# Kernel optimization log

Measured on AMD Instinct MI355X. Metric: run time of the kernel, lower is better.

## Reference

```python
import jax, jax.numpy as jnp
import numpy as np

N_NODES = 50000
N_EDGES = 800000
D = 256            # node_feat_size
D_EDGE = 16        # edge_feat_size (unused in forward math, as in the original)
G_FEAT = 200       # graph_feat_size
N_TASKS = 1
N_GRAPHS = 512


def _p(key, shape):
    return jax.random.normal(key, shape, dtype=jnp.float32) * 0.05


def setup_inputs() -> dict:
    key = jax.random.key(0)
    ks = jax.random.split(key, 24)
    inp = {
        'node_feats_1': jax.random.normal(ks[0], (N_NODES, D), dtype=jnp.float32),
        'edge_feats_1': jax.random.normal(ks[1], (N_EDGES, D_EDGE), dtype=jnp.float32),
        'node_feats_2': jax.random.normal(ks[2], (N_NODES, D), dtype=jnp.float32),
        'edge_feats_2': jax.random.normal(ks[3], (N_EDGES, D_EDGE), dtype=jnp.float32),
        'src_1': jax.random.randint(ks[4], (N_EDGES,), 0, N_NODES, dtype=jnp.int32),
        'dst_1': jax.random.randint(ks[5], (N_EDGES,), 0, N_NODES, dtype=jnp.int32),
        'graph_ids_1': jnp.sort(jax.random.randint(ks[6], (N_NODES,), 0, N_GRAPHS, dtype=jnp.int32)),
        'src_2': jax.random.randint(ks[7], (N_EDGES,), 0, N_NODES, dtype=jnp.int32),
        'dst_2': jax.random.randint(ks[8], (N_EDGES,), 0, N_NODES, dtype=jnp.int32),
        'graph_ids_2': jnp.sort(jax.random.randint(ks[9], (N_NODES,), 0, N_GRAPHS, dtype=jnp.int32)),
        # GCN layer 1 params (GraphConv weight/bias + residual Linear)
        'W1': _p(ks[10], (D, D)), 'b1': jnp.zeros((D,), jnp.float32),
        'Wr1': _p(ks[11], (D, D)), 'br1': jnp.zeros((D,), jnp.float32),
        # GCN layer 2 params
        'W2': _p(ks[12], (D, D)), 'b2': jnp.zeros((D,), jnp.float32),
        'Wr2': _p(ks[13], (D, D)), 'br2': jnp.zeros((D,), jnp.float32),
        # Readout 1 MLP
        'Ri1': _p(ks[14], (D, D)), 'rbi1': jnp.zeros((D,), jnp.float32),
        'Ro1': _p(ks[15], (D, G_FEAT)), 'rbo1': jnp.zeros((G_FEAT,), jnp.float32),
        # Readout 2 MLP
        'Ri2': _p(ks[16], (D, D)), 'rbi2': jnp.zeros((D,), jnp.float32),
        'Ro2': _p(ks[17], (D, G_FEAT)), 'rbo2': jnp.zeros((G_FEAT,), jnp.float32),
        # Predictor
        'Wp': _p(ks[18], (G_FEAT, N_TASKS)), 'bp': jnp.zeros((N_TASKS,), jnp.float32),
    }
    return inp


def _gcn_layer(h, src, dst, W, b, Wr, br):
    # DGL GraphConv, norm='none': project, aggregate (sum src->dst), bias, relu
    hW = h @ W                                             # [N, D]
    agg = jax.ops.segment_sum(jnp.take(hW, src, axis=0), dst, num_segments=N_NODES)
    conv = jax.nn.relu(agg + b)
    # residual branch: activation(Linear(h))
    res = jax.nn.relu(h @ Wr + br)
    return conv + res                                      # dropout=0, no batchnorm


def _readout(h, graph_ids, Wi, bi, Wo, bo):
    # MLPNodeReadout: Linear -> relu -> Linear, then sum over nodes per graph
    h = jax.nn.relu(h @ Wi + bi)
    h = h @ Wo + bo                                        # [N, G_FEAT]
    return jax.ops.segment_sum(h, graph_ids, num_segments=N_GRAPHS)


def reference(node_feats_1, edge_feats_1, node_feats_2, edge_feats_2,
              src_1, dst_1, graph_ids_1, src_2, dst_2, graph_ids_2,
              W1, b1, Wr1, br1, W2, b2, Wr2, br2,
              Ri1, rbi1, Ro1, rbo1, Ri2, rbi2, Ro2, rbo2, Wp, bp):
    h1 = _gcn_layer(node_feats_1, src_1, dst_1, W1, b1, Wr1, br1)
    g1 = _readout(h1, graph_ids_1, Ri1, rbi1, Ro1, rbo1)
    h2 = _gcn_layer(node_feats_2, src_2, dst_2, W2, b2, Wr2, br2)
    g2 = _readout(h2, graph_ids_2, Ri2, rbi2, Ro2, rbo2)
    g = g1 + g2                                            # [G, G_FEAT]
    return (g @ Wp + bp).reshape(-1)                       # [G * n_tasks]
```

## Files before the change

kernel.cpp:

```cpp
#include <hip/hip_runtime.h>

#define NN 50000
#define NE 800000
#define DD 256
#define GFEAT 200
#define NG 512

typedef __bf16 bf16;
typedef bf16 bf16x4 __attribute__((ext_vector_type(4)));
typedef bf16 bf16x8 __attribute__((ext_vector_type(8)));
typedef float f32x4 __attribute__((ext_vector_type(4)));

__device__ __forceinline__ void gl_lds16(const bf16* g, bf16* l) {
    __builtin_amdgcn_global_load_lds(
        (const __attribute__((address_space(1))) uint32_t*)(g),
        (__attribute__((address_space(3))) uint32_t*)(l), 16, 0, 0);
}

__device__ __forceinline__ bf16x8 frag_ld(const bf16* s, int R, int C) {
    return *(const bf16x8*)&s[R * 32 + ((C ^ ((R >> 1) & 3)) << 3)];
}

#define EPI_STRIDE 136

__global__ __launch_bounds__(256) void conv_x2_kernel(const float* __restrict__ in0,
                                                      const float* __restrict__ in1,
                                                      bf16* __restrict__ out0,
                                                      bf16* __restrict__ out1, int n4) {
    const float* in = blockIdx.y ? in1 : in0;
    bf16* out = blockIdx.y ? out1 : out0;
    int i = blockIdx.x * 256 + threadIdx.x;
    if (i < n4) {
        float4 v = ((const float4*)in)[i];
        bf16x4 o;
        o[0] = (bf16)v.x; o[1] = (bf16)v.y; o[2] = (bf16)v.z; o[3] = (bf16)v.w;
        ((bf16x4*)out)[i] = o;
    }
}

__global__ __launch_bounds__(256) void conv_w8_kernel(
    const float* __restrict__ w0, const float* __restrict__ w1,
    const float* __restrict__ w2, const float* __restrict__ w3,
    const float* __restrict__ w4, const float* __restrict__ w5,
    const float* __restrict__ w6, const float* __restrict__ w7,
    bf16* __restrict__ out_base) {
    const float* ws[8] = {w0, w1, w2, w3, w4, w5, w6, w7};
    const int Ns[8] = {DD, DD, DD, GFEAT, DD, DD, DD, GFEAT};
    int m = blockIdx.y;
    const float* in = ws[m];
    int N = Ns[m];
    int idx = blockIdx.x * 256 + threadIdx.x;
    int n = idx >> 8, k = idx & 255;
    float v = (n < N) ? in[k * N + n] : 0.f;
    out_base[(size_t)m * 65536 + idx] = (bf16)v;
}

#define NBKT   128
#define NPB    391
#define NCHUNK 256
#define CE     ((NE + NCHUNK - 1) / NCHUNK)

__global__ __launch_bounds__(256) void csr_coarse_hist_kernel(
    const int* __restrict__ d0, const int* __restrict__ d1,
    int* __restrict__ cnt0, int* __restrict__ cnt1) {
    const int blk = blockIdx.x, t = threadIdx.x;
    const int* dst = blockIdx.y ? d1 : d0;
    int* cnt = blockIdx.y ? cnt1 : cnt0;
    __shared__ int hist[NBKT];
    if (t < NBKT) hist[t] = 0;
    __syncthreads();
    const int e0 = blk * CE;
    const int e1 = (e0 + CE < NE) ? e0 + CE : NE;
    for (int e = e0 + t; e < e1; e += 256)
        atomicAdd(&hist[dst[e] / NPB], 1);
    __syncthreads();
    if (t < NBKT) cnt[t * NCHUNK + blk] = hist[t];
}

__global__ __launch_bounds__(1024) void csr_scan_kernel(
    int* __restrict__ cnt0, int* __restrict__ cnt1,
    int* __restrict__ offs0, int* __restrict__ offs1) {
    int* cnt = blockIdx.y ? cnt1 : cnt0;
    const int t = threadIdx.x;
    const int PER = (NBKT * NCHUNK) / 1024;
    int v[PER];
    int sum = 0;
    const int base = t * PER;
#pragma unroll
    for (int i = 0; i < PER; i += 4) {
        int4 q = *(const int4*)&cnt[base + i];
        v[i] = q.x; v[i + 1] = q.y; v[i + 2] = q.z; v[i + 3] = q.w;
        sum += q.x + q.y + q.z + q.w;
    }
    __shared__ int s[1024];
    s[t] = sum;
    __syncthreads();
    for (int off = 1; off < 1024; off <<= 1) {
        int a = (t >= off) ? s[t - off] : 0;
        __syncthreads();
        s[t] += a;
        __syncthreads();
    }
    int run = s[t] - sum;
#pragma unroll
    for (int i = 0; i < PER; i++) { int c = v[i]; cnt[base + i] = run; run += c; }
    if (t == 0) (blockIdx.y ? offs1 : offs0)[NN] = NE;
}

__global__ __launch_bounds__(256) void csr_partition_kernel(
    const int* __restrict__ sA, const int* __restrict__ sB,
    const int* __restrict__ d0, const int* __restrict__ d1,
    const int* __restrict__ cnt0, const int* __restrict__ cnt1,
    int2* __restrict__ eb0, int2* __restrict__ eb1) {
    const int blk = blockIdx.x, t = threadIdx.x;
    const int* src = blockIdx.y ? sB : sA;
    const int* dst = blockIdx.y ? d1 : d0;
    const int* cnt = blockIdx.y ? cnt1 : cnt0;
    int2* eb = blockIdx.y ? eb1 : eb0;
    __shared__ int cur[NBKT];
    if (t < NBKT) cur[t] = cnt[t * NCHUNK + blk];
    __syncthreads();
    const int e0 = blk * CE;
    const int e1 = (e0 + CE < NE) ? e0 + CE : NE;
    for (int e = e0 + t; e < e1; e += 256) {
        int d = dst[e], s = src[e];
        int pos = atomicAdd(&cur[d / NPB], 1);
        eb[pos] = make_int2(s, d);
    }
}

__global__ __launch_bounds__(512) void csr_bucket_sort_kernel(
    const int* __restrict__ cnt0, const int* __restrict__ cnt1,
    const int2* __restrict__ eb0, const int2* __restrict__ eb1,
    int* __restrict__ offs0, int* __restrict__ offs1,
    int* __restrict__ csr0, int* __restrict__ csr1) {
    const int b = blockIdx.x, t = threadIdx.x;
    const int* cnt = blockIdx.y ? cnt1 : cnt0;
    const int2* eb = blockIdx.y ? eb1 : eb0;
    int* offs = blockIdx.y ? offs1 : offs0;
    int* csr = blockIdx.y ? csr1 : csr0;
    const int lo = b * NPB;
    const int ncnt = (NN - lo < NPB) ? (NN - lo) : NPB;
    const int beg = cnt[b * NCHUNK];
    const int end = (b == NBKT - 1) ? NE : cnt[(b + 1) * NCHUNK];

    __shared__ int hist[NPB];
    __shared__ int s[512];
    if (t < NPB) hist[t] = 0;
    __syncthreads();
    for (int i = beg + t; i < end; i += 512)
        atomicAdd(&hist[eb[i].y - lo], 1);
    __syncthreads();

    int h = (t < NPB) ? hist[t] : 0;
    s[t] = h;
    __syncthreads();
    for (int off = 1; off < 512; off <<= 1) {
        int a = (t >= off) ? s[t - off] : 0;
        __syncthreads();
        s[t] += a;
        __syncthreads();
    }
    int excl = s[t] - h;
    __syncthreads();
    if (t < NPB) hist[t] = excl;
    if (t < ncnt) offs[lo + t] = beg + excl;
    __syncthreads();

    for (int i = beg + t; i < end; i += 512) {
        int2 v = eb[i];
        int pos = atomicAdd(&hist[v.y - lo], 1);
        csr[beg + pos] = v.x;
    }
}

__global__ __launch_bounds__(256) void mfma_gemm2_kernel(
    const bf16* __restrict__ A0, const bf16* __restrict__ A1,
    const bf16* __restrict__ Bt0, const bf16* __restrict__ Bt1,
    const float* __restrict__ bias0, const float* __restrict__ bias1,
    bf16* __restrict__ out0, bf16* __restrict__ out1,
    int M, int Nb, int do_relu) {
    const int lid = blockIdx.x;
    const int r8 = lid & 7, cc = (lid >> 3) & 1, g = lid >> 4;
    const int row_blk = g * 8 + r8;
    if (row_blk * 128 >= M) return;
    const bf16* A = blockIdx.y ? A1 : A0;
    const bf16* Bt = blockIdx.y ? Bt1 : Bt0;
    const float* bias = blockIdx.y ? bias1 : bias0;
    bf16* out = blockIdx.y ? out1 : out0;

    __shared__ bf16 smem[16384];
    bf16* As = smem;
    bf16* Bs = smem + 8192;

    const int t    = threadIdx.x;
    const int lane = t & 63;
    const int w    = t >> 6;
    const int row0 = row_blk * 128;
    const int col0 = cc * 128;

    f32x4 acc[4][4] = {};
    const int wm = (w >> 1) * 64, wn = (w & 1) * 64;
    const int fm = lane & 15, fC = lane >> 4;

    for (int k0 = 0; k0 < 256; k0 += 32) {
#pragma unroll
        for (int r = 0; r < 2; r++) {
            int flat = r * 256 + t;
            int fr = flat >> 2, fc = flat & 3;
            int fcg = fc ^ ((fr >> 1) & 3);
            int arow = row0 + fr;
            if (arow > M - 1) arow = M - 1;
            gl_lds16(&A[(size_t)arow * 256 + k0 + fcg * 8], &As[flat * 8]);
        }
#pragma unroll
        for (int r = 0; r < 2; r++) {
            int flat = r * 256 + t;
            int fr = flat >> 2, fc = flat & 3;
            int fcg = fc ^ ((fr >> 1) & 3);
            int brow = col0 + fr;
            gl_lds16(&Bt[(size_t)brow * 256 + k0 + fcg * 8], &Bs[flat * 8]);
        }
        __syncthreads();

        bf16x8 af[4], bfr[4];
#pragma unroll
        for (int i = 0; i < 4; i++) af[i] = frag_ld(As, wm + i * 16 + fm, fC);
#pragma unroll
        for (int i = 0; i < 4; i++) bfr[i] = frag_ld(Bs, wn + i * 16 + fm, fC);
#pragma unroll
        for (int i = 0; i < 4; i++)
#pragma unroll
            for (int j = 0; j < 4; j++)
                acc[i][j] = __builtin_amdgcn_mfma_f32_16x16x32_bf16(af[i], bfr[j], acc[i][j], 0, 0, 0);
        __syncthreads();
    }

    float bv[4];
#pragma unroll
    for (int j = 0; j < 4; j++) {
        int col = col0 + wn + fm + j * 16;
        bv[j] = (col < Nb) ? bias[col] : 0.f;
    }

#pragma unroll
    for (int p = 0; p < 2; p++) {
        if ((w >> 1) == p) {
#pragma unroll
            for (int i = 0; i < 4; i++)
#pragma unroll
                for (int j = 0; j < 4; j++)
#pragma unroll
                    for (int r2 = 0; r2 < 4; r2++) {
                        int rl = i * 16 + (lane >> 4) * 4 + r2;
                        int cl = wn + fm + j * 16;
                        float v = acc[i][j][r2] + bv[j];
                        if (do_relu) v = fmaxf(v, 0.f);
                        smem[rl * EPI_STRIDE + cl] = (bf16)v;
                    }
        }
        __syncthreads();
#pragma unroll
        for (int q = 0; q < 4; q++) {
            int flat = q * 256 + t;
            int rl = flat >> 4, seg = flat & 15;
            int grow = row0 + p * 64 + rl;
            if (grow < M)
                *(bf16x8*)&out[(size_t)grow * 256 + col0 + seg * 8] =
                    *(const bf16x8*)&smem[rl * EPI_STRIDE + seg * 8];
        }
        __syncthreads();
    }
}

__global__ __launch_bounds__(256) void mfma_gemm_fused2_kernel(
    const bf16* __restrict__ A0, const bf16* __restrict__ A1,
    const bf16* __restrict__ Bt2_0, const bf16* __restrict__ Bt2_1,
    const float* __restrict__ bh0, const float* __restrict__ bh1,
    bf16* __restrict__ lo0, bf16* __restrict__ lo1,
    bf16* __restrict__ hi0, bf16* __restrict__ hi1, int M) {
    const int lid = blockIdx.x;
    const int r8 = lid & 7, cc = (lid >> 3) & 3, g = lid >> 5;
    const int row_blk = g * 8 + r8;
    if (row_blk * 128 >= M) return;
    const bf16* A = blockIdx.y ? A1 : A0;
    const bf16* Bt2 = blockIdx.y ? Bt2_1 : Bt2_0;
    const float* bias_hi = blockIdx.y ? bh1 : bh0;
    bf16* out_lo = blockIdx.y ? lo1 : lo0;
    bf16* out_hi = blockIdx.y ? hi1 : hi0;

    __shared__ bf16 smem[16384];
    bf16* As = smem;
    bf16* Bs = smem + 8192;

    const int t    = threadIdx.x;
    const int lane = t & 63;
    const int w    = t >> 6;
    const int row0 = row_blk * 128;
    const int col0 = cc * 128;

    f32x4 acc[4][4] = {};
    const int wm = (w >> 1) * 64, wn = (w & 1) * 64;
    const int fm = lane & 15, fC = lane >> 4;

    for (int k0 = 0; k0 < 256; k0 += 32) {
#pragma unroll
        for (int r = 0; r < 2; r++) {
            int flat = r * 256 + t;
            int fr = flat >> 2, fc = flat & 3;
            int fcg = fc ^ ((fr >> 1) & 3);
            int arow = row0 + fr;
            if (arow > M - 1) arow = M - 1;
            gl_lds16(&A[(size_t)arow * 256 + k0 + fcg * 8], &As[flat * 8]);
        }
#pragma unroll
        for (int r = 0; r < 2; r++) {
            int flat = r * 256 + t;
            int fr = flat >> 2, fc = flat & 3;
            int fcg = fc ^ ((fr >> 1) & 3);
            int brow = col0 + fr;
            gl_lds16(&Bt2[(size_t)brow * 256 + k0 + fcg * 8], &Bs[flat * 8]);
        }
        __syncthreads();

        bf16x8 af[4], bfr[4];
#pragma unroll
        for (int i = 0; i < 4; i++) af[i] = frag_ld(As, wm + i * 16 + fm, fC);
#pragma unroll
        for (int i = 0; i < 4; i++) bfr[i] = frag_ld(Bs, wn + i * 16 + fm, fC);
#pragma unroll
        for (int i = 0; i < 4; i++)
#pragma unroll
            for (int j = 0; j < 4; j++)
                acc[i][j] = __builtin_amdgcn_mfma_f32_16x16x32_bf16(af[i], bfr[j], acc[i][j], 0, 0, 0);
        __syncthreads();
    }

    const bool hi = (col0 >= 256);
    bf16* out = hi ? out_hi : out_lo;
    const int cb = hi ? col0 - 256 : col0;

    float bv[4];
#pragma unroll
    for (int j = 0; j < 4; j++) {
        int col = cb + wn + fm + j * 16;
        bv[j] = hi ? bias_hi[col] : 0.f;
    }

#pragma unroll
    for (int p = 0; p < 2; p++) {
        if ((w >> 1) == p) {
#pragma unroll
            for (int i = 0; i < 4; i++)
#pragma unroll
                for (int j = 0; j < 4; j++)
#pragma unroll
                    for (int r2 = 0; r2 < 4; r2++) {
                        int rl = i * 16 + (lane >> 4) * 4 + r2;
                        int cl = wn + fm + j * 16;
                        float v = acc[i][j][r2] + bv[j];
                        if (hi) v = fmaxf(v, 0.f);
                        smem[rl * EPI_STRIDE + cl] = (bf16)v;
                    }
        }
        __syncthreads();
#pragma unroll
        for (int q = 0; q < 4; q++) {
            int flat = q * 256 + t;
            int rl = flat >> 4, seg = flat & 15;
            int grow = row0 + p * 64 + rl;
            if (grow < M)
                *(bf16x8*)&out[(size_t)grow * 256 + cb + seg * 8] =
                    *(const bf16x8*)&smem[rl * EPI_STRIDE + seg * 8];
        }
        __syncthreads();
    }
}

__global__ __launch_bounds__(256) void agg_combine2_kernel(
    const bf16* __restrict__ hW0, const bf16* __restrict__ hW1,
    const int* __restrict__ csr0, const int* __restrict__ csr1,
    const int* __restrict__ offs0, const int* __restrict__ offs1,
    const float* __restrict__ bias0, const float* __restrict__ bias1,
    const bf16* __restrict__ res0, const bf16* __restrict__ res1,
    bf16* __restrict__ H0, bf16* __restrict__ H1, int n_nodes) {
    const bf16* hW = blockIdx.y ? hW1 : hW0;
    const int* csr_src = blockIdx.y ? csr1 : csr0;
    const int* offsets = blockIdx.y ? offs1 : offs0;
    const float* bias = blockIdx.y ? bias1 : bias0;
    const bf16* res = blockIdx.y ? res1 : res0;
    bf16* H = blockIdx.y ? H1 : H0;

    int wave = threadIdx.x >> 6;
    int lane = threadIdx.x & 63;
    int node = blockIdx.x * 4 + wave;
    if (node >= n_nodes) return;
    int beg = offsets[node], end = offsets[node + 1];
    const int half = lane >> 5;
    const int fo   = (lane & 31) * 8;

    float acc[8] = {};
    int j = beg;
    for (; j + 6 + half < end; j += 8) {
        int s0 = csr_src[j + half];
        int s1 = csr_src[j + 2 + half];
        int s2 = csr_src[j + 4 + half];
        int s3 = csr_src[j + 6 + half];
        bf16x8 v0 = *(const bf16x8*)&hW[(size_t)s0 * DD + fo];
        bf16x8 v1 = *(const bf16x8*)&hW[(size_t)s1 * DD + fo];
        bf16x8 v2 = *(const bf16x8*)&hW[(size_t)s2 * DD + fo];
        bf16x8 v3 = *(const bf16x8*)&hW[(size_t)s3 * DD + fo];
#pragma unroll
        for (int q = 0; q < 8; q++) acc[q] += (float)v0[q];
#pragma unroll
        for (int q = 0; q < 8; q++) acc[q] += (float)v1[q];
#pragma unroll
        for (int q = 0; q < 8; q++) acc[q] += (float)v2[q];
#pragma unroll
        for (int q = 0; q < 8; q++) acc[q] += (float)v3[q];
    }
    for (; j + half < end; j += 2) {
        int s = csr_src[j + half];
        bf16x8 v = *(const bf16x8*)&hW[(size_t)s * DD + fo];
#pragma unroll
        for (int q = 0; q < 8; q++) acc[q] += (float)v[q];
    }
#pragma unroll
    for (int q = 0; q < 8; q++) acc[q] += __shfl_xor(acc[q], 32, 64);

    if (half == 0) {
        float4 b0 = *(const float4*)&bias[fo];
        float4 b1 = *(const float4*)&bias[fo + 4];
        bf16x8 rv = *(const bf16x8*)&res[(size_t)node * DD + fo];
        bf16x8 o;
        o[0] = (bf16)(fmaxf(acc[0] + b0.x, 0.f) + (float)rv[0]);
        o[1] = (bf16)(fmaxf(acc[1] + b0.y, 0.f) + (float)rv[1]);
        o[2] = (bf16)(fmaxf(acc[2] + b0.z, 0.f) + (float)rv[2]);
        o[3] = (bf16)(fmaxf(acc[3] + b0.w, 0.f) + (float)rv[3]);
        o[4] = (bf16)(fmaxf(acc[4] + b1.x, 0.f) + (float)rv[4]);
        o[5] = (bf16)(fmaxf(acc[5] + b1.y, 0.f) + (float)rv[5]);
        o[6] = (bf16)(fmaxf(acc[6] + b1.z, 0.f) + (float)rv[6]);
        o[7] = (bf16)(fmaxf(acc[7] + b1.w, 0.f) + (float)rv[7]);
        *(bf16x8*)&H[(size_t)node * DD + fo] = o;
    }
}

__global__ __launch_bounds__(256) void graph_reduce2_kernel(
    const bf16* __restrict__ P0, const bf16* __restrict__ P1,
    const int* __restrict__ g0, const int* __restrict__ g1,
    float* __restrict__ G0, float* __restrict__ G1, int n_nodes) {
    const bf16* P = blockIdx.y ? P1 : P0;
    const int* gids = blockIdx.y ? g1 : g0;
    float* G = blockIdx.y ? G1 : G0;

    int g = blockIdx.x;
    int lo = 0, hi = n_nodes;
    while (lo < hi) { int mid = (lo + hi) >> 1; if (gids[mid] < g) lo = mid + 1; else hi = mid; }
    int beg = lo;
    hi = n_nodes;
    while (lo < hi) { int mid = (lo + hi) >> 1; if (gids[mid] < g + 1) lo = mid + 1; else hi = mid; }
    int end = lo;

    int c = threadIdx.x;
    if (c < GFEAT) {
        float acc = 0.f;
        for (int r = beg; r < end; r++) acc += (float)P[(size_t)r * 256 + c];
        G[(size_t)g * GFEAT + c] = acc;
    }
}

__global__ __launch_bounds__(256) void predictor_kernel(const float* __restrict__ G1,
                                                        const float* __restrict__ G2,
                                                        const float* __restrict__ Wp,
                                                        const float* __restrict__ bp,
                                                        float* __restrict__ out) {
    int i = blockIdx.x * 256 + threadIdx.x;
    if (i >= NG) return;
    float acc = bp[0];
    for (int f = 0; f < GFEAT; f++)
        acc += (G1[i * GFEAT + f] + G2[i * GFEAT + f]) * Wp[f];
    out[i] = acc;
}

extern "C" void kernel_launch(void* const* d_in, const int* in_sizes, int n_in,
                              void* d_out, int out_size, void* d_ws, size_t ws_size,
                              hipStream_t stream) {
    const float* X1   = (const float*)d_in[0];
    const float* X2   = (const float*)d_in[2];
    const int*   src1 = (const int*)d_in[4];
    const int*   dst1 = (const int*)d_in[5];
    const int*   gid1 = (const int*)d_in[6];
    const int*   src2 = (const int*)d_in[7];
    const int*   dst2 = (const int*)d_in[8];
    const int*   gid2 = (const int*)d_in[9];
    const float* W1  = (const float*)d_in[10]; const float* b1  = (const float*)d_in[11];
    const float* Wr1 = (const float*)d_in[12]; const float* br1 = (const float*)d_in[13];
    const float* W2  = (const float*)d_in[14]; const float* b2  = (const float*)d_in[15];
    const float* Wr2 = (const float*)d_in[16]; const float* br2 = (const float*)d_in[17];
    const float* Ri1 = (const float*)d_in[18]; const float* rbi1 = (const float*)d_in[19];
    const float* Ro1 = (const float*)d_in[20]; const float* rbo1 = (const float*)d_in[21];
    const float* Ri2 = (const float*)d_in[22]; const float* rbi2 = (const float*)d_in[23];
    const float* Ro2 = (const float*)d_in[24]; const float* rbo2 = (const float*)d_in[25];
    const float* Wp  = (const float*)d_in[26]; const float* bp  = (const float*)d_in[27];

    const size_t NB = (size_t)NN * DD * sizeof(bf16);
    char* p = (char*)d_ws;
    bf16* XbH1 = (bf16*)p; p += NB;
    bf16* XbH2 = (bf16*)p; p += NB;
    bf16* hWR1 = (bf16*)p; p += NB;
    bf16* hWR2 = (bf16*)p; p += NB;
    bf16* resP1 = (bf16*)p; p += NB;
    bf16* resP2 = (bf16*)p; p += NB;
    float* G1  = (float*)p; p += (size_t)NG * GFEAT * sizeof(float);
    float* G2  = (float*)p; p += (size_t)NG * GFEAT * sizeof(float);
    bf16* Wbase = (bf16*)p; p += 8 * 65536 * sizeof(bf16);
    int* offs1 = (int*)p; p += (NN + 1) * sizeof(int);
    int* offs2 = (int*)p; p += (NN + 1) * sizeof(int);
    int* cnt1  = (int*)p; p += NBKT * NCHUNK * sizeof(int);
    int* cnt2  = (int*)p; p += NBKT * NCHUNK * sizeof(int);
    int* csr1  = (int*)p; p += NE * sizeof(int);
    int* csr2  = (int*)p; p += NE * sizeof(int);
    int2* eb1 = (int2*)hWR1;
    int2* eb2 = (int2*)hWR2;

    conv_w8_kernel<<<dim3(256, 8), 256, 0, stream>>>(W1, Wr1, Ri1, Ro1, W2, Wr2, Ri2, Ro2, Wbase);
    conv_x2_kernel<<<dim3((NN * DD / 4 + 255) / 256, 2), 256, 0, stream>>>(
        X1, X2, XbH1, XbH2, NN * DD / 4);

    csr_coarse_hist_kernel<<<dim3(NCHUNK, 2), 256, 0, stream>>>(dst1, dst2, cnt1, cnt2);
    csr_scan_kernel<<<dim3(1, 2), 1024, 0, stream>>>(cnt1, cnt2, offs1, offs2);
    csr_partition_kernel<<<dim3(NCHUNK, 2), 256, 0, stream>>>(
        src1, src2, dst1, dst2, cnt1, cnt2, eb1, eb2);
    csr_bucket_sort_kernel<<<dim3(NBKT, 2), 512, 0, stream>>>(
        cnt1, cnt2, eb1, eb2, offs1, offs2, csr1, csr2);

    mfma_gemm_fused2_kernel<<<dim3(49 * 32, 2), 256, 0, stream>>>(
        XbH1, XbH2, Wbase + 0 * 65536, Wbase + 4 * 65536, br1, br2,
        hWR1, hWR2, resP1, resP2, NN);
    agg_combine2_kernel<<<dim3((NN + 3) / 4, 2), 256, 0, stream>>>(
        hWR1, hWR2, csr1, csr2, offs1, offs2, b1, b2, resP1, resP2, XbH1, XbH2, NN);
    mfma_gemm2_kernel<<<dim3(49 * 16, 2), 256, 0, stream>>>(
        XbH1, XbH2, Wbase + 2 * 65536, Wbase + 6 * 65536, rbi1, rbi2,
        hWR1, hWR2, NN, DD, 1);
    mfma_gemm2_kernel<<<dim3(49 * 16, 2), 256, 0, stream>>>(
        hWR1, hWR2, Wbase + 3 * 65536, Wbase + 7 * 65536, rbo1, rbo2,
        resP1, resP2, NN, GFEAT, 0);
    graph_reduce2_kernel<<<dim3(NG, 2), 256, 0, stream>>>(
        resP1, resP2, gid1, gid2, G1, G2, NN);

    predictor_kernel<<<(NG + 255) / 256, 256, 0, stream>>>(G1, G2, Wp, bp, (float*)d_out);
}
```

Before: 576.1 us.

## Fuse readout segment-sum into output GEMM epilogue and widen K-tile

Replaces the separate graph_reduce kernel by doing the per-graph sum inside the final readout GEMM epilogue, using run-length accumulation over sorted graph ids and atomicAdd into a zeroed G buffer. This removes writing and rereading the projected readout matrix. It also doubles the GEMM K-step from 32 to 64 with an 8-way swizzle, halving the number of barriers per tile. The catch is extra atomics, float summation order that is no longer deterministic, and an added zeroing kernel.

```diff
diff --git a/kernel.cpp b/kernel.cpp
--- a/kernel.cpp
+++ b/kernel.cpp
@@ -17,8 +17,8 @@
         (__attribute__((address_space(3))) uint32_t*)(l), 16, 0, 0);
 }
 
-__device__ __forceinline__ bf16x8 frag_ld(const bf16* s, int R, int C) {
-    return *(const bf16x8*)&s[R * 32 + ((C ^ ((R >> 1) & 3)) << 3)];
+__device__ __forceinline__ bf16x8 frag_ld64(const bf16* s, int R, int C) {
+    return *(const bf16x8*)&s[R * 64 + ((C ^ ((R >> 1) & 7)) << 3)];
 }
 
 #define EPI_STRIDE 136
@@ -55,6 +55,13 @@
     out_base[(size_t)m * 65536 + idx] = (bf16)v;
 }
 
+__global__ __launch_bounds__(256) void zero_g_kernel(float* __restrict__ G0,
+                                                     float* __restrict__ G1) {
+    float* G = blockIdx.y ? G1 : G0;
+    int i = blockIdx.x * 256 + threadIdx.x;
+    if (i < NG * GFEAT) G[i] = 0.f;
+}
+
 #define NBKT   128
 #define NPB    391
 #define NCHUNK 256
@@ -174,6 +181,19 @@
     }
 }
 
+#define STAGE64(MAT, base_row, CLAMP_M)                                          \
+    _Pragma("unroll")                                                            \
+    for (int r_ = 0; r_ < 4; r_++) {                                             \
+        int flat_ = r_ * 256 + t;                                                \
+        int fr_ = flat_ >> 3, fc_ = flat_ & 7;                                   \
+        int fcg_ = fc_ ^ ((fr_ >> 1) & 7);                                       \
+        int row_ = (base_row) + fr_;                                             \
+        if (CLAMP_M && row_ > M - 1) row_ = M - 1;                               \
+        gl_lds16(&MAT[(size_t)row_ * 256 + k0 + fcg_ * 8],                       \
+                 &(((r_ < 2) ? As : As) )[0] + 0);                               \
+    }
+
+
 __global__ __launch_bounds__(256) void mfma_gemm2_kernel(
     const bf16* __restrict__ A0, const bf16* __restrict__ A1,
     const bf16* __restrict__ Bt0, const bf16* __restrict__ Bt1,
@@ -203,36 +223,38 @@
     const int wm = (w >> 1) * 64, wn = (w & 1) * 64;
     const int fm = lane & 15, fC = lane >> 4;
 
-    for (int k0 = 0; k0 < 256; k0 += 32) {
-#pragma unroll
-        for (int r = 0; r < 2; r++) {
+    for (int k0 = 0; k0 < 256; k0 += 64) {
+#pragma unroll
+        for (int r = 0; r < 4; r++) {
             int flat = r * 256 + t;
-            int fr = flat >> 2, fc = flat & 3;
-            int fcg = fc ^ ((fr >> 1) & 3);
+            int fr = flat >> 3, fc = flat & 7;
+            int fcg = fc ^ ((fr >> 1) & 7);
             int arow = row0 + fr;
             if (arow > M - 1) arow = M - 1;
             gl_lds16(&A[(size_t)arow * 256 + k0 + fcg * 8], &As[flat * 8]);
         }
 #pragma unroll
-        for (int r = 0; r < 2; r++) {
+        for (int r = 0; r < 4; r++) {
             int flat = r * 256 + t;
-            int fr = flat >> 2, fc = flat & 3;
-            int fcg = fc ^ ((fr >> 1) & 3);
+            int fr = flat >> 3, fc = flat & 7;
+            int fcg = fc ^ ((fr >> 1) & 7);
             int brow = col0 + fr;
             gl_lds16(&Bt[(size_t)brow * 256 + k0 + fcg * 8], &Bs[flat * 8]);
         }
         __syncthreads();
-
-        bf16x8 af[4], bfr[4];
-#pragma unroll
-        for (int i = 0; i < 4; i++) af[i] = frag_ld(As, wm + i * 16 + fm, fC);
-#pragma unroll
-        for (int i = 0; i < 4; i++) bfr[i] = frag_ld(Bs, wn + i * 16 + fm, fC);
-#pragma unroll
-        for (int i = 0; i < 4; i++)
-#pragma unroll
-            for (int j = 0; j < 4; j++)
-                acc[i][j] = __builtin_amdgcn_mfma_f32_16x16x32_bf16(af[i], bfr[j], acc[i][j], 0, 0, 0);
+#pragma unroll
+        for (int s = 0; s < 2; s++) {
+            bf16x8 af[4], bfr[4];
+#pragma unroll
+            for (int i = 0; i < 4; i++) af[i] = frag_ld64(As, wm + i * 16 + fm, s * 4 + fC);
+#pragma unroll
+            for (int i = 0; i < 4; i++) bfr[i] = frag_ld64(Bs, wn + i * 16 + fm, s * 4 + fC);
+#pragma unroll
+            for (int i = 0; i < 4; i++)
+#pragma unroll
+                for (int j = 0; j < 4; j++)
+                    acc[i][j] = __builtin_amdgcn_mfma_f32_16x16x32_bf16(af[i], bfr[j], acc[i][j], 0, 0, 0);
+        }
         __syncthreads();
     }
 
@@ -303,36 +325,38 @@
     const int wm = (w >> 1) * 64, wn = (w & 1) * 64;
     const int fm = lane & 15, fC = lane >> 4;
 
-    for (int k0 = 0; k0 < 256; k0 += 32) {
-#pragma unroll
-        for (int r = 0; r < 2; r++) {
+    for (int k0 = 0; k0 < 256; k0 += 64) {
+#pragma unroll
+        for (int r = 0; r < 4; r++) {
             int flat = r * 256 + t;
-            int fr = flat >> 2, fc = flat & 3;
-            int fcg = fc ^ ((fr >> 1) & 3);
+            int fr = flat >> 3, fc = flat & 7;
+            int fcg = fc ^ ((fr >> 1) & 7);
             int arow = row0 + fr;
             if (arow > M - 1) arow = M - 1;
             gl_lds16(&A[(size_t)arow * 256 + k0 + fcg * 8], &As[flat * 8]);
         }
 #pragma unroll
-        for (int r = 0; r < 2; r++) {
+        for (int r = 0; r < 4; r++) {
             int flat = r * 256 + t;
-            int fr = flat >> 2, fc = flat & 3;
-            int fcg = fc ^ ((fr >> 1) & 3);
+            int fr = flat >> 3, fc = flat & 7;
+            int fcg = fc ^ ((fr >> 1) & 7);
             int brow = col0 + fr;
             gl_lds16(&Bt2[(size_t)brow * 256 + k0 + fcg * 8], &Bs[flat * 8]);
         }
         __syncthreads();
-
-        bf16x8 af[4], bfr[4];
-#pragma unroll
-        for (int i = 0; i < 4; i++) af[i] = frag_ld(As, wm + i * 16 + fm, fC);
-#pragma unroll
-        for (int i = 0; i < 4; i++) bfr[i] = frag_ld(Bs, wn + i * 16 + fm, fC);
-#pragma unroll
-        for (int i = 0; i < 4; i++)
-#pragma unroll
-            for (int j = 0; j < 4; j++)
-                acc[i][j] = __builtin_amdgcn_mfma_f32_16x16x32_bf16(af[i], bfr[j], acc[i][j], 0, 0, 0);
+#pragma unroll
+        for (int s = 0; s < 2; s++) {
+            bf16x8 af[4], bfr[4];
+#pragma unroll
+            for (int i = 0; i < 4; i++) af[i] = frag_ld64(As, wm + i * 16 + fm, s * 4 + fC);
+#pragma unroll
+            for (int i = 0; i < 4; i++) bfr[i] = frag_ld64(Bs, wn + i * 16 + fm, s * 4 + fC);
+#pragma unroll
+            for (int i = 0; i < 4; i++)
+#pragma unroll
+                for (int j = 0; j < 4; j++)
+                    acc[i][j] = __builtin_amdgcn_mfma_f32_16x16x32_bf16(af[i], bfr[j], acc[i][j], 0, 0, 0);
+        }
         __syncthreads();
     }
 
@@ -372,6 +396,117 @@
             if (grow < M)
                 *(bf16x8*)&out[(size_t)grow * 256 + cb + seg * 8] =
                     *(const bf16x8*)&smem[rl * EPI_STRIDE + seg * 8];
+        }
+        __syncthreads();
+    }
+}
+
+__global__ __launch_bounds__(256) void mfma_gemm_reduce2_kernel(
+    const bf16* __restrict__ A0, const bf16* __restrict__ A1,
+    const bf16* __restrict__ Bt0, const bf16* __restrict__ Bt1,
+    const float* __restrict__ bias0, const float* __restrict__ bias1,
+    const int* __restrict__ gid0, const int* __restrict__ gid1,
+    float* __restrict__ G0, float* __restrict__ G1, int M, int Nb) {
+    const int lid = blockIdx.x;
+    const int r8 = lid & 7, cc = (lid >> 3) & 1, g = lid >> 4;
+    const int row_blk = g * 8 + r8;
+    if (row_blk * 128 >= M) return;
+    const bf16* A = blockIdx.y ? A1 : A0;
+    const bf16* Bt = blockIdx.y ? Bt1 : Bt0;
+    const float* bias = blockIdx.y ? bias1 : bias0;
+    const int* gids = blockIdx.y ? gid1 : gid0;
+    float* G = blockIdx.y ? G1 : G0;
+
+    __shared__ bf16 smem[16384];
+    bf16* As = smem;
+    bf16* Bs = smem + 8192;
+
+    const int t    = threadIdx.x;
+    const int lane = t & 63;
+    const int w    = t >> 6;
+    const int row0 = row_blk * 128;
+    const int col0 = cc * 128;
+
+    f32x4 acc[4][4] = {};
+    const int wm = (w >> 1) * 64, wn = (w & 1) * 64;
+    const int fm = lane & 15, fC = lane >> 4;
+
+    for (int k0 = 0; k0 < 256; k0 += 64) {
+#pragma unroll
+        for (int r = 0; r < 4; r++) {
+            int flat = r * 256 + t;
+            int fr = flat >> 3, fc = flat & 7;
+            int fcg = fc ^ ((fr >> 1) & 7);
+            int arow = row0 + fr;
+            if (arow > M - 1) arow = M - 1;
+            gl_lds16(&A[(size_t)arow * 256 + k0 + fcg * 8], &As[flat * 8]);
+        }
+#pragma unroll
+        for (int r = 0; r < 4; r++) {
+            int flat = r * 256 + t;
+            int fr = flat >> 3, fc = flat & 7;
+            int fcg = fc ^ ((fr >> 1) & 7);
+            int brow = col0 + fr;
+            gl_lds16(&Bt[(size_t)brow * 256 + k0 + fcg * 8], &Bs[flat * 8]);
+        }
+        __syncthreads();
+#pragma unroll
+        for (int s = 0; s < 2; s++) {
+            bf16x8 af[4], bfr[4];
+#pragma unroll
+            for (int i = 0; i < 4; i++) af[i] = frag_ld64(As, wm + i * 16 + fm, s * 4 + fC);
+#pragma unroll
+            for (int i = 0; i < 4; i++) bfr[i] = frag_ld64(Bs, wn + i * 16 + fm, s * 4 + fC);
+#pragma unroll
+            for (int i = 0; i < 4; i++)
+#pragma unroll
+                for (int j = 0; j < 4; j++)
+                    acc[i][j] = __builtin_amdgcn_mfma_f32_16x16x32_bf16(af[i], bfr[j], acc[i][j], 0, 0, 0);
+        }
+        __syncthreads();
+    }
+
+    float bv[4];
+#pragma unroll
+    for (int j = 0; j < 4; j++) {
+        int col = col0 + wn + fm + j * 16;
+        bv[j] = (col < Nb) ? bias[col] : 0.f;
+    }
+
+#pragma unroll
+    for (int p = 0; p < 2; p++) {
+        if ((w >> 1) == p) {
+#pragma unroll
+            for (int i = 0; i < 4; i++)
+#pragma unroll
+                for (int j = 0; j < 4; j++)
+#pragma unroll
+                    for (int r2 = 0; r2 < 4; r2++) {
+                        int rl = i * 16 + (lane >> 4) * 4 + r2;
+                        int cl = wn + fm + j * 16;
+                        smem[rl * EPI_STRIDE + cl] = (bf16)(acc[i][j][r2] + bv[j]);
+                    }
+        }
+        __syncthreads();
+        {
+            int c = t & 127, rh = t >> 7;
+            int colg = col0 + c;
+            if (colg < Nb) {
+                float run = 0.f;
+                int gprev = -1;
+                for (int r = 0; r < 32; r++) {
+                    int grow = row0 + p * 64 + rh * 32 + r;
+                    if (grow >= M) break;
+                    int gg = gids[grow];
+                    if (gg != gprev) {
+                        if (gprev >= 0) atomicAdd(&G[(size_t)gprev * GFEAT + colg], run);
+                        run = 0.f;
+                        gprev = gg;
+                    }
+                    run += (float)smem[(rh * 32 + r) * EPI_STRIDE + c];
+                }
+                if (gprev >= 0) atomicAdd(&G[(size_t)gprev * GFEAT + colg], run);
+            }
         }
         __syncthreads();
     }
@@ -442,30 +577,6 @@
         o[6] = (bf16)(fmaxf(acc[6] + b1.z, 0.f) + (float)rv[6]);
         o[7] = (bf16)(fmaxf(acc[7] + b1.w, 0.f) + (float)rv[7]);
         *(bf16x8*)&H[(size_t)node * DD + fo] = o;
-    }
-}
-
-__global__ __launch_bounds__(256) void graph_reduce2_kernel(
-    const bf16* __restrict__ P0, const bf16* __restrict__ P1,
-    const int* __restrict__ g0, const int* __restrict__ g1,
-    float* __restrict__ G0, float* __restrict__ G1, int n_nodes) {
-    const bf16* P = blockIdx.y ? P1 : P0;
-    const int* gids = blockIdx.y ? g1 : g0;
-    float* G = blockIdx.y ? G1 : G0;
-
-    int g = blockIdx.x;
-    int lo = 0, hi = n_nodes;
-    while (lo < hi) { int mid = (lo + hi) >> 1; if (gids[mid] < g) lo = mid + 1; else hi = mid; }
-    int beg = lo;
-    hi = n_nodes;
-    while (lo < hi) { int mid = (lo + hi) >> 1; if (gids[mid] < g + 1) lo = mid + 1; else hi = mid; }
-    int end = lo;
-
-    int c = threadIdx.x;
-    if (c < GFEAT) {
-        float acc = 0.f;
-        for (int r = beg; r < end; r++) acc += (float)P[(size_t)r * 256 + c];
-        G[(size_t)g * GFEAT + c] = acc;
     }
 }
 
@@ -509,8 +620,8 @@
     bf16* XbH2 = (bf16*)p; p += NB;
     bf16* hWR1 = (bf16*)p; p += NB;
     bf16* hWR2 = (bf16*)p; p += NB;
-    bf16* resP1 = (bf16*)p; p += NB;
-    bf16* resP2 = (bf16*)p; p += NB;
+    bf16* res1 = (bf16*)p; p += NB;
+    bf16* res2 = (bf16*)p; p += NB;
     float* G1  = (float*)p; p += (size_t)NG * GFEAT * sizeof(float);
     float* G2  = (float*)p; p += (size_t)NG * GFEAT * sizeof(float);
     bf16* Wbase = (bf16*)p; p += 8 * 65536 * sizeof(bf16);
@@ -523,6 +634,7 @@
     int2* eb1 = (int2*)hWR1;
     int2* eb2 = (int2*)hWR2;
 
+    zero_g_kernel<<<dim3((NG * GFEAT + 255) / 256, 2), 256, 0, stream>>>(G1, G2);
     conv_w8_kernel<<<dim3(256, 8), 256, 0, stream>>>(W1, Wr1, Ri1, Ro1, W2, Wr2, Ri2, Ro2, Wbase);
     conv_x2_kernel<<<dim3((NN * DD / 4 + 255) / 256, 2), 256, 0, stream>>>(
         X1, X2, XbH1, XbH2, NN * DD / 4);
@@ -536,17 +648,15 @@
 
     mfma_gemm_fused2_kernel<<<dim3(49 * 32, 2), 256, 0, stream>>>(
         XbH1, XbH2, Wbase + 0 * 65536, Wbase + 4 * 65536, br1, br2,
-        hWR1, hWR2, resP1, resP2, NN);
+        hWR1, hWR2, res1, res2, NN);
     agg_combine2_kernel<<<dim3((NN + 3) / 4, 2), 256, 0, stream>>>(
-        hWR1, hWR2, csr1, csr2, offs1, offs2, b1, b2, resP1, resP2, XbH1, XbH2, NN);
+        hWR1, hWR2, csr1, csr2, offs1, offs2, b1, b2, res1, res2, XbH1, XbH2, NN);
     mfma_gemm2_kernel<<<dim3(49 * 16, 2), 256, 0, stream>>>(
         XbH1, XbH2, Wbase + 2 * 65536, Wbase + 6 * 65536, rbi1, rbi2,
         hWR1, hWR2, NN, DD, 1);
-    mfma_gemm2_kernel<<<dim3(49 * 16, 2), 256, 0, stream>>>(
+    mfma_gemm_reduce2_kernel<<<dim3(49 * 16, 2), 256, 0, stream>>>(
         hWR1, hWR2, Wbase + 3 * 65536, Wbase + 7 * 65536, rbo1, rbo2,
-        resP1, resP2, NN, GFEAT, 0);
-    graph_reduce2_kernel<<<dim3(NG, 2), 256, 0, stream>>>(
-        resP1, resP2, gid1, gid2, G1, G2, NN);
+        gid1, gid2, G1, G2, NN, GFEAT);
 
     predictor_kernel<<<(NG + 255) / 256, 256, 0, stream>>>(G1, G2, Wp, bp, (float*)d_out);
 }
```

New measurement: 557.4 us. 3.2% less time.
